# Performance work log

Measured on AMD Instinct MI355X. Metric: run time of the kernel, lower is better.

The kernel has to match this reference:

```python
import jax, jax.numpy as jnp
import numpy as np

B, C, H, W = 8, 256, 48, 48
G = 32  # num_groups
EPS = 1e-5


def setup_inputs() -> dict:
    key = jax.random.key(0)
    ks = jax.random.split(key, 9)
    s = 0.02
    return {
        "input": jax.random.normal(ks[0], (B, C, H, W), dtype=jnp.float32),
        "Wq": jax.random.normal(ks[1], (C, C), dtype=jnp.float32) * s,
        "bq": jnp.zeros((C,), dtype=jnp.float32),
        "Wk": jax.random.normal(ks[2], (C, C), dtype=jnp.float32) * s,
        "bk": jnp.zeros((C,), dtype=jnp.float32),
        "Wv": jax.random.normal(ks[3], (C, C), dtype=jnp.float32) * s,
        "bv": jnp.zeros((C,), dtype=jnp.float32),
        "gn_w": jnp.ones((C,), dtype=jnp.float32),
        "gn_b": jnp.zeros((C,), dtype=jnp.float32),
    }


def _group_norm(x, w, b):
    # x: [B, C, H, W] -> normalize per (group) over (C//G, H, W)
    n, c, h, wd = x.shape
    xg = x.reshape(n, G, c // G, h, wd)
    mean = jnp.mean(xg, axis=(2, 3, 4), keepdims=True)
    var = jnp.var(xg, axis=(2, 3, 4), keepdims=True)
    xg = (xg - mean) * jax.lax.rsqrt(var + EPS)
    x = xg.reshape(n, c, h, wd)
    return x * w[None, :, None, None] + b[None, :, None, None]


def _conv1x1(x, wgt, bias):
    # 1x1 conv == per-pixel channel GEMM. wgt: [C_out, C_in]
    return jnp.einsum('bchw,oc->bohw', x, wgt) + bias[None, :, None, None]


def reference(input, Wq, bq, Wk, bk, Wv, bv, gn_w, gn_b):
    x = _group_norm(input, gn_w, gn_b)
    q = _conv1x1(x, Wq, bq)
    k = _conv1x1(x, Wk, bk)
    v = _conv1x1(x, Wv, bv)
    d = q.shape[1]
    # energy[b,h,w,h',w'] = sum_c q[b,c,h,w] * k[b,c,h',w'] / sqrt(d)
    energy = jnp.einsum('bchw,bcef->bhwef', q, k) / jnp.sqrt(jnp.float32(d))
    n, h, w2 = energy.shape[0], energy.shape[1], energy.shape[2]
    energy = jax.nn.softmax(energy.reshape(n, h, w2, h * w2), axis=-1)
    energy = energy.reshape(n, h, w2, h, w2)
    # out[b,c,h,w] = sum_{h',w'} energy[b,h,w,h',w'] * v[b,c,h',w']
    out = jnp.einsum('bhwef,bcef->bchw', energy, v)
    return out
```

## Files before the change

kernel.cpp:

```cpp
#include <hip/hip_runtime.h>
#include <math.h>

#define NB 8
#define NC 256
#define NHW 2304
#define NG 32
#define CPG 8
#define GN_EPS 1e-5f
#define ATT_SCALE 0.0625f
#define XSTR 258

typedef __bf16 bf16x8 __attribute__((ext_vector_type(8)));
typedef __bf16 bf16x4 __attribute__((ext_vector_type(4)));
typedef float f32x4 __attribute__((ext_vector_type(4)));

#define MFMA(a, b, c) __builtin_amdgcn_mfma_f32_16x16x32_bf16(a, b, c, 0, 0, 0)

__device__ __forceinline__ void async_lds16(const void* g, void* l) {
  __builtin_amdgcn_global_load_lds(
      (const __attribute__((address_space(1))) void*)g,
      (__attribute__((address_space(3))) void*)l, 16, 0, 0);
}

__global__ __launch_bounds__(256) void k_prep(
    const float* __restrict__ x, const float* __restrict__ gn_w,
    const float* __restrict__ gn_b, float* __restrict__ scale,
    float* __restrict__ shift,
    const float* __restrict__ Wq, const float* __restrict__ Wk,
    const float* __restrict__ Wv, __bf16* __restrict__ Wqb,
    __bf16* __restrict__ Wkb, __bf16* __restrict__ Wvb) {
  __shared__ float red[8];
  int blk = blockIdx.x;
  if (blk >= 256) {
    int idx = blk - 256;
    int which = idx >> 6;
    const float* src = which == 0 ? Wq : (which == 1 ? Wk : Wv);
    __bf16* dst = which == 0 ? Wqb : (which == 1 ? Wkb : Wvb);
    int i = (idx & 63) * 256 + threadIdx.x;
    float4 v = ((const float4*)src)[i];
    bf16x4 o;
    o[0] = (__bf16)v.x; o[1] = (__bf16)v.y;
    o[2] = (__bf16)v.z; o[3] = (__bf16)v.w;
    ((bf16x4*)dst)[i] = o;
    return;
  }
  const float4* base = (const float4*)(x + (size_t)blk * CPG * NHW);
  const int n4 = CPG * NHW / 4;
  float s = 0.f, ss = 0.f;
  for (int i = threadIdx.x; i < n4; i += 256) {
    float4 v = base[i];
    s  += v.x + v.y + v.z + v.w;
    ss += v.x * v.x + v.y * v.y + v.z * v.z + v.w * v.w;
  }
  for (int off = 32; off > 0; off >>= 1) {
    s  += __shfl_down(s, off);
    ss += __shfl_down(ss, off);
  }
  int wv = threadIdx.x >> 6, ln = threadIdx.x & 63;
  if (ln == 0) { red[wv] = s; red[4 + wv] = ss; }
  __syncthreads();
  if (threadIdx.x < CPG) {
    float S  = red[0] + red[1] + red[2] + red[3];
    float SS = red[4] + red[5] + red[6] + red[7];
    const float inv_n = 1.f / (float)(CPG * NHW);
    float mean = S * inv_n;
    float var  = SS * inv_n - mean * mean;
    float rstd = rsqrtf(var + GN_EPS);
    int b = blk / NG, g = blk % NG;
    int c = g * CPG + threadIdx.x;
    float sc = gn_w[c] * rstd;
    scale[b * NC + c] = sc;
    shift[b * NC + c] = gn_b[c] - mean * sc;
  }
}

__global__ __launch_bounds__(256) void k_xnT(
    const float* __restrict__ x, const float* __restrict__ scale,
    const float* __restrict__ shift, __bf16* __restrict__ xnT) {
  __shared__ __bf16 t[64 * XSTR];
  int p0 = blockIdx.x * 64;
  int b = blockIdx.y;
  int w = threadIdx.x >> 6, lane = threadIdx.x & 63;
  const float* xb = x + (size_t)b * NC * NHW;
  const float* scb = scale + b * NC;
  const float* shb = shift + b * NC;
#pragma unroll 8
  for (int i = 0; i < 64; ++i) {
    int c = i * 4 + w;
    float v = xb[(size_t)c * NHW + p0 + lane] * scb[c] + shb[c];
    t[lane * XSTR + c] = (__bf16)v;
  }
  __syncthreads();
#pragma unroll
  for (int i = 0; i < 8; ++i) {
    int row = i * 8 + w * 2 + (lane >> 5);
    int c8 = (lane & 31) * 8;
    bf16x8 v8 = *(const bf16x8*)&t[row * XSTR + c8];
    *(bf16x8*)&xnT[((size_t)b * NHW + p0 + row) * NC + c8] = v8;
  }
}

__global__ __launch_bounds__(256) void k_qkv(
    const __bf16* __restrict__ xnT,
    const __bf16* __restrict__ Wqb, const __bf16* __restrict__ Wkb,
    const __bf16* __restrict__ Wvb,
    const float* __restrict__ bq, const float* __restrict__ bk,
    const float* __restrict__ bv,
    __bf16* __restrict__ qT, __bf16* __restrict__ kT,
    __bf16* __restrict__ vbuf) {
  __shared__ __bf16 tile[9216];
  int blk = blockIdx.x;
  int b = blk & 7;
  int r = blk >> 3;
  int oq = r & 3;
  int pg = r >> 2;
  int p0 = pg * 128, o0 = oq * 64;
  int tid = threadIdx.x;
  int w = tid >> 6, lane = tid & 63;
  int col = lane & 15, quad = lane >> 4;

  const __bf16* xrow =
      xnT + ((size_t)b * NHW + p0 + w * 32 + col) * NC + quad * 8;
  bf16x8 xf[2][8];
#pragma unroll
  for (int mt = 0; mt < 2; ++mt)
#pragma unroll
    for (int ks = 0; ks < 8; ++ks)
      xf[mt][ks] = *(const bf16x8*)(xrow + (size_t)mt * 16 * NC + ks * 32);

#pragma unroll
  for (int t = 0; t < 3; ++t) {
    const __bf16* W = t == 0 ? Wqb : (t == 1 ? Wkb : Wvb);
    const float* bias = t == 0 ? bq : (t == 1 ? bk : bv);
    f32x4 acc[2][4];
#pragma unroll
    for (int mt = 0; mt < 2; ++mt)
#pragma unroll
      for (int nt = 0; nt < 4; ++nt) acc[mt][nt] = (f32x4){0.f, 0.f, 0.f, 0.f};
#pragma unroll
    for (int nt = 0; nt < 4; ++nt) {
      const __bf16* wrow = W + ((size_t)(o0 + nt * 16 + col)) * NC + quad * 8;
#pragma unroll
      for (int ks = 0; ks < 8; ++ks) {
        bf16x8 wf = *(const bf16x8*)(wrow + ks * 32);
        acc[0][nt] = MFMA(xf[0][ks], wf, acc[0][nt]);
        acc[1][nt] = MFMA(xf[1][ks], wf, acc[1][nt]);
      }
    }
    if (t > 0) __syncthreads();
    if (t < 2) {
#pragma unroll
      for (int mt = 0; mt < 2; ++mt)
#pragma unroll
        for (int nt = 0; nt < 4; ++nt) {
          float bc = bias[o0 + nt * 16 + col];
#pragma unroll
          for (int reg = 0; reg < 4; ++reg) {
            int row = w * 32 + mt * 16 + quad * 4 + reg;
            tile[row * 72 + nt * 16 + col] = (__bf16)(acc[mt][nt][reg] + bc);
          }
        }
      __syncthreads();
      __bf16* dst = t == 0 ? qT : kT;
#pragma unroll
      for (int pass = 0; pass < 4; ++pass) {
        int unit = pass * 256 + tid;
        int row = unit >> 3, ch = unit & 7;
        bf16x8 v8 = *(const bf16x8*)&tile[row * 72 + ch * 8];
        *(bf16x8*)&dst[((size_t)b * NHW + p0 + row) * NC + o0 + ch * 8] = v8;
      }
    } else {
#pragma unroll
      for (int mt = 0; mt < 2; ++mt)
#pragma unroll
        for (int nt = 0; nt < 4; ++nt) {
          float bc = bias[o0 + nt * 16 + col];
#pragma unroll
          for (int reg = 0; reg < 4; ++reg) {
            int p = w * 32 + mt * 16 + quad * 4 + reg;
            tile[(nt * 16 + col) * 136 + p] = (__bf16)(acc[mt][nt][reg] + bc);
          }
        }
      __syncthreads();
#pragma unroll
      for (int pass = 0; pass < 4; ++pass) {
        int unit = pass * 256 + tid;
        int row = unit >> 4, ch = unit & 15;
        bf16x8 v8 = *(const bf16x8*)&tile[row * 136 + ch * 8];
        *(bf16x8*)&vbuf[((size_t)b * NC + o0 + row) * NHW + p0 + ch * 8] = v8;
      }
    }
  }
}

__global__ __launch_bounds__(256, 2) void k_fused(
    const __bf16* __restrict__ qT, const __bf16* __restrict__ kT,
    const __bf16* __restrict__ vbuf, float* __restrict__ out) {
  __shared__ __bf16 sk[64 * 256];
  __shared__ __bf16 sv[256 * 64];
  __shared__ __bf16 sp[64 * 64];
  __shared__ float slsum[2][64];

  int blk = blockIdx.x;
  int b = blk & 7;
  int qg = blk >> 3;
  int q0 = qg * 64;
  int tid = threadIdx.x;
  int w = tid >> 6, lane = tid & 63;
  int wm = w >> 1, wn = w & 1;
  int col = lane & 15, quad = lane >> 4;
  int c7 = col & 7;

  auto stage_kv = [&](int it2) {
    int k0 = it2 * 64;
    {
      int sub = lane >> 5, p5 = lane & 31;
#pragma unroll
      for (int j = 0; j < 8; ++j) {
        int r0 = w * 16 + j * 2;
        int rloc = r0 + sub;
        int g = p5 ^ (rloc & 7);
        async_lds16(kT + ((size_t)b * NHW + k0 + rloc) * NC + g * 8,
                    (void*)&sk[r0 * 256]);
      }
    }
    {
      int sub = lane >> 3, p3 = lane & 7;
#pragma unroll
      for (int j = 0; j < 8; ++j) {
        int r0 = w * 64 + j * 8;
        int rloc = r0 + sub;
        int g = p3 ^ (rloc & 7);
        async_lds16(vbuf + ((size_t)b * NC + rloc) * NHW + k0 + g * 8,
                    (void*)&sv[r0 * 64]);
      }
    }
  };

  const __bf16* qrow =
      qT + ((size_t)b * NHW + q0 + wn * 32 + col) * NC + quad * 8;
  bf16x8 qf[2][8];
#pragma unroll
  for (int nt = 0; nt < 2; ++nt)
#pragma unroll
    for (int ks = 0; ks < 8; ++ks)
      qf[nt][ks] = *(const bf16x8*)(qrow + (size_t)nt * 16 * NC + ks * 32);

  stage_kv(0);

  f32x4 acc[4][4];
#pragma unroll
  for (int mt = 0; mt < 4; ++mt)
#pragma unroll
    for (int nt = 0; nt < 4; ++nt) acc[mt][nt] = (f32x4){0.f, 0.f, 0.f, 0.f};
  float lsum_r[2] = {0.f, 0.f};

  for (int it = 0; it < 36; ++it) {
    __syncthreads();

    f32x4 sacc[2][2];
#pragma unroll
    for (int mt = 0; mt < 2; ++mt)
#pragma unroll
      for (int nt = 0; nt < 2; ++nt) sacc[mt][nt] = (f32x4){0.f, 0.f, 0.f, 0.f};
#pragma unroll
    for (int ks = 0; ks < 8; ++ks) {
#pragma unroll
      for (int mt = 0; mt < 2; ++mt) {
        int krow = wm * 32 + mt * 16 + col;
        bf16x8 kf = *(const bf16x8*)
            &sk[krow * 256 + (((ks * 4 + quad) ^ c7) << 3)];
        sacc[mt][0] = MFMA(kf, qf[0][ks], sacc[mt][0]);
        sacc[mt][1] = MFMA(kf, qf[1][ks], sacc[mt][1]);
      }
    }

#pragma unroll
    for (int nt = 0; nt < 2; ++nt) {
      float ps = 0.f;
      int q = wn * 32 + nt * 16 + col;
#pragma unroll
      for (int mt = 0; mt < 2; ++mt) {
        bf16x4 pk;
#pragma unroll
        for (int reg = 0; reg < 4; ++reg) {
          float e = __expf(sacc[mt][nt][reg] * ATT_SCALE);
          ps += e;
          pk[reg] = (__bf16)e;
        }
        int chunk = (wm * 4 + mt * 2 + (quad >> 1)) ^ c7;
        *(bf16x4*)&sp[q * 64 + chunk * 8 + (quad & 1) * 4] = pk;
      }
      ps += __shfl_xor(ps, 16);
      ps += __shfl_xor(ps, 32);
      lsum_r[nt] += ps;
    }

    __syncthreads();

    bf16x8 pf[4][2], vf[4][2];
#pragma unroll
    for (int nt = 0; nt < 4; ++nt) {
      int q = nt * 16 + col;
#pragma unroll
      for (int ks = 0; ks < 2; ++ks)
        pf[nt][ks] = *(const bf16x8*)
            &sp[q * 64 + (((ks * 4 + quad) ^ c7) << 3)];
    }
#pragma unroll
    for (int mt = 0; mt < 4; ++mt) {
      int crow = w * 64 + mt * 16 + col;
#pragma unroll
      for (int ks = 0; ks < 2; ++ks)
        vf[mt][ks] = *(const bf16x8*)
            &sv[crow * 64 + (((ks * 4 + quad) ^ c7) << 3)];
    }
    if (it < 35) {
      asm volatile("s_waitcnt lgkmcnt(0)" ::: "memory");
      __builtin_amdgcn_sched_barrier(0);
      stage_kv(it + 1);
    }

#pragma unroll
    for (int mt = 0; mt < 4; ++mt)
#pragma unroll
      for (int nt = 0; nt < 4; ++nt) {
        acc[mt][nt] = MFMA(vf[mt][0], pf[nt][0], acc[mt][nt]);
        acc[mt][nt] = MFMA(vf[mt][1], pf[nt][1], acc[mt][nt]);
      }
  }

  if (quad == 0) {
#pragma unroll
    for (int nt = 0; nt < 2; ++nt)
      slsum[wm][wn * 32 + nt * 16 + col] = lsum_r[nt];
  }
  __syncthreads();

  float* ob = out + (size_t)b * NC * NHW;
#pragma unroll
  for (int nt = 0; nt < 4; ++nt) {
    int q = nt * 16 + col;
    float inv = 1.f / (slsum[0][q] + slsum[1][q]);
#pragma unroll
    for (int mt = 0; mt < 4; ++mt) {
#pragma unroll
      for (int reg = 0; reg < 4; ++reg) {
        int c = w * 64 + mt * 16 + quad * 4 + reg;
        ob[(size_t)c * NHW + q0 + q] = acc[mt][nt][reg] * inv;
      }
    }
  }
}

extern "C" void kernel_launch(void* const* d_in, const int* in_sizes, int n_in,
                              void* d_out, int out_size, void* d_ws,
                              size_t ws_size, hipStream_t stream) {
  const float* x   = (const float*)d_in[0];
  const float* Wq  = (const float*)d_in[1];
  const float* bq  = (const float*)d_in[2];
  const float* Wk  = (const float*)d_in[3];
  const float* bk  = (const float*)d_in[4];
  const float* Wv  = (const float*)d_in[5];
  const float* bv  = (const float*)d_in[6];
  const float* gnw = (const float*)d_in[7];
  const float* gnb = (const float*)d_in[8];
  float* out = (float*)d_out;

  const size_t per = (size_t)NB * NC * NHW;
  const size_t psz = (size_t)NB * NHW * NHW * 2;
  char* wsb = (char*)d_ws;
  __bf16* qT   = (__bf16*)wsb;
  __bf16* kT   = (__bf16*)(wsb + per * 2);
  __bf16* vbuf = (__bf16*)(wsb + per * 4);
  __bf16* xnT  = (__bf16*)(wsb + per * 6);
  char* tail   = wsb + per * 6 + psz;
  __bf16* Wqb  = (__bf16*)tail;
  __bf16* Wkb  = Wqb + NC * NC;
  __bf16* Wvb  = Wkb + NC * NC;
  float* scale = (float*)(Wvb + NC * NC);
  float* shift = scale + NB * NC;

  hipLaunchKernelGGL(k_prep, dim3(448), dim3(256), 0, stream,
                     x, gnw, gnb, scale, shift, Wq, Wk, Wv, Wqb, Wkb, Wvb);
  hipLaunchKernelGGL(k_xnT, dim3(NHW / 64, NB), dim3(256), 0, stream,
                     x, scale, shift, xnT);
  hipLaunchKernelGGL(k_qkv, dim3(576), dim3(256), 0, stream,
                     xnT, Wqb, Wkb, Wvb, bq, bk, bv, qT, kT, vbuf);
  hipLaunchKernelGGL(k_fused, dim3(288), dim3(256), 0, stream,
                     qT, kT, vbuf, out);
}
```

Baseline: 243.6 us.

## Restructure fused attention: 32-query tiles, Q in LDS, K/V direct from global

The fused attention kernel now processes 32 queries per block instead of 64, doubling the grid to 576 blocks and raising the occupancy target to 3 blocks per CU. Q is staged once into swizzled LDS, while K and V fragments are loaded straight from global memory into registers each iteration instead of through async LDS staging. A double-buffered P tile replaces one of the two per-iteration block barriers. This aims to improve occupancy and cut LDS traffic and synchronisation, at the cost of reading K/V from global (or L2) more often, with no explicit prefetch overlap.

After: 329.2 us. +35.2%, slower.

```diff
diff --git a/kernel.cpp b/kernel.cpp
--- a/kernel.cpp
+++ b/kernel.cpp
@@ -15,12 +15,6 @@
 typedef float f32x4 __attribute__((ext_vector_type(4)));
 
 #define MFMA(a, b, c) __builtin_amdgcn_mfma_f32_16x16x32_bf16(a, b, c, 0, 0, 0)
-
-__device__ __forceinline__ void async_lds16(const void* g, void* l) {
-  __builtin_amdgcn_global_load_lds(
-      (const __attribute__((address_space(1))) void*)g,
-      (__attribute__((address_space(3))) void*)l, 16, 0, 0);
-}
 
 __global__ __launch_bounds__(256) void k_prep(
     const float* __restrict__ x, const float* __restrict__ gn_w,
@@ -193,155 +187,117 @@
   }
 }
 
-__global__ __launch_bounds__(256, 2) void k_fused(
+__global__ __launch_bounds__(256, 3) void k_fused(
     const __bf16* __restrict__ qT, const __bf16* __restrict__ kT,
     const __bf16* __restrict__ vbuf, float* __restrict__ out) {
-  __shared__ __bf16 sk[64 * 256];
-  __shared__ __bf16 sv[256 * 64];
-  __shared__ __bf16 sp[64 * 64];
-  __shared__ float slsum[2][64];
+  __shared__ __bf16 sq[32 * 256];
+  __shared__ __bf16 sp[2][32 * 64];
+  __shared__ float slsum[4][32];
 
   int blk = blockIdx.x;
   int b = blk & 7;
   int qg = blk >> 3;
-  int q0 = qg * 64;
+  int q0 = qg * 32;
   int tid = threadIdx.x;
   int w = tid >> 6, lane = tid & 63;
-  int wm = w >> 1, wn = w & 1;
   int col = lane & 15, quad = lane >> 4;
   int c7 = col & 7;
 
-  auto stage_kv = [&](int it2) {
-    int k0 = it2 * 64;
-    {
-      int sub = lane >> 5, p5 = lane & 31;
-#pragma unroll
-      for (int j = 0; j < 8; ++j) {
-        int r0 = w * 16 + j * 2;
-        int rloc = r0 + sub;
-        int g = p5 ^ (rloc & 7);
-        async_lds16(kT + ((size_t)b * NHW + k0 + rloc) * NC + g * 8,
-                    (void*)&sk[r0 * 256]);
-      }
-    }
-    {
-      int sub = lane >> 3, p3 = lane & 7;
-#pragma unroll
-      for (int j = 0; j < 8; ++j) {
-        int r0 = w * 64 + j * 8;
-        int rloc = r0 + sub;
-        int g = p3 ^ (rloc & 7);
-        async_lds16(vbuf + ((size_t)b * NC + rloc) * NHW + k0 + g * 8,
-                    (void*)&sv[r0 * 64]);
-      }
-    }
-  };
-
-  const __bf16* qrow =
-      qT + ((size_t)b * NHW + q0 + wn * 32 + col) * NC + quad * 8;
-  bf16x8 qf[2][8];
-#pragma unroll
-  for (int nt = 0; nt < 2; ++nt)
+  {
+    const __bf16* qb = qT + ((size_t)b * NHW + q0) * NC;
+#pragma unroll
+    for (int pass = 0; pass < 4; ++pass) {
+      int unit = pass * 256 + tid;
+      int q = unit >> 5, ch = unit & 31;
+      bf16x8 v8 = *(const bf16x8*)(qb + q * NC + ch * 8);
+      *(bf16x8*)&sq[q * 256 + ((ch ^ (q & 7)) << 3)] = v8;
+    }
+  }
+  __syncthreads();
+
+  const __bf16* kbase = kT + ((size_t)b * NHW + w * 16 + col) * NC + quad * 8;
+  const __bf16* vbase =
+      vbuf + ((size_t)b * NC + w * 64 + col) * NHW + quad * 8;
+
+  f32x4 acc[4][2];
+#pragma unroll
+  for (int mt = 0; mt < 4; ++mt)
+#pragma unroll
+    for (int nt = 0; nt < 2; ++nt) acc[mt][nt] = (f32x4){0.f, 0.f, 0.f, 0.f};
+  float lsum_r[2] = {0.f, 0.f};
+
+  for (int it = 0; it < 36; ++it) {
+    const __bf16* kp = kbase + (size_t)it * 64 * NC;
+    bf16x8 kf[8];
 #pragma unroll
     for (int ks = 0; ks < 8; ++ks)
-      qf[nt][ks] = *(const bf16x8*)(qrow + (size_t)nt * 16 * NC + ks * 32);
-
-  stage_kv(0);
-
-  f32x4 acc[4][4];
-#pragma unroll
-  for (int mt = 0; mt < 4; ++mt)
-#pragma unroll
-    for (int nt = 0; nt < 4; ++nt) acc[mt][nt] = (f32x4){0.f, 0.f, 0.f, 0.f};
-  float lsum_r[2] = {0.f, 0.f};
-
-  for (int it = 0; it < 36; ++it) {
-    __syncthreads();
-
-    f32x4 sacc[2][2];
-#pragma unroll
-    for (int mt = 0; mt < 2; ++mt)
-#pragma unroll
-      for (int nt = 0; nt < 2; ++nt) sacc[mt][nt] = (f32x4){0.f, 0.f, 0.f, 0.f};
+      kf[ks] = *(const bf16x8*)(kp + ks * 32);
+    const __bf16* vp = vbase + it * 64;
+    bf16x8 vf[4][2];
+#pragma unroll
+    for (int mt = 0; mt < 4; ++mt)
+#pragma unroll
+      for (int ks = 0; ks < 2; ++ks)
+        vf[mt][ks] = *(const bf16x8*)(vp + (size_t)mt * 16 * NHW + ks * 32);
+
+    f32x4 sacc[2];
+    sacc[0] = (f32x4){0.f, 0.f, 0.f, 0.f};
+    sacc[1] = (f32x4){0.f, 0.f, 0.f, 0.f};
 #pragma unroll
     for (int ks = 0; ks < 8; ++ks) {
-#pragma unroll
-      for (int mt = 0; mt < 2; ++mt) {
-        int krow = wm * 32 + mt * 16 + col;
-        bf16x8 kf = *(const bf16x8*)
-            &sk[krow * 256 + (((ks * 4 + quad) ^ c7) << 3)];
-        sacc[mt][0] = MFMA(kf, qf[0][ks], sacc[mt][0]);
-        sacc[mt][1] = MFMA(kf, qf[1][ks], sacc[mt][1]);
-      }
-    }
-
+      int sl = ((ks * 4 + quad) ^ c7) << 3;
+      bf16x8 q0f = *(const bf16x8*)&sq[col * 256 + sl];
+      bf16x8 q1f = *(const bf16x8*)&sq[(16 + col) * 256 + sl];
+      sacc[0] = MFMA(kf[ks], q0f, sacc[0]);
+      sacc[1] = MFMA(kf[ks], q1f, sacc[1]);
+    }
+
+    __bf16* spc = sp[it & 1];
+    int wrch = w * 2 + (quad >> 1);
 #pragma unroll
     for (int nt = 0; nt < 2; ++nt) {
       float ps = 0.f;
-      int q = wn * 32 + nt * 16 + col;
-#pragma unroll
-      for (int mt = 0; mt < 2; ++mt) {
-        bf16x4 pk;
-#pragma unroll
-        for (int reg = 0; reg < 4; ++reg) {
-          float e = __expf(sacc[mt][nt][reg] * ATT_SCALE);
-          ps += e;
-          pk[reg] = (__bf16)e;
-        }
-        int chunk = (wm * 4 + mt * 2 + (quad >> 1)) ^ c7;
-        *(bf16x4*)&sp[q * 64 + chunk * 8 + (quad & 1) * 4] = pk;
-      }
+      bf16x4 pk;
+#pragma unroll
+      for (int reg = 0; reg < 4; ++reg) {
+        float e = __expf(sacc[nt][reg] * ATT_SCALE);
+        ps += e;
+        pk[reg] = (__bf16)e;
+      }
+      int q = nt * 16 + col;
+      *(bf16x4*)&spc[q * 64 + ((wrch ^ c7) << 3) + (quad & 1) * 4] = pk;
       ps += __shfl_xor(ps, 16);
       ps += __shfl_xor(ps, 32);
       lsum_r[nt] += ps;
     }
-
-    __syncthreads();
-
-    bf16x8 pf[4][2], vf[4][2];
-#pragma unroll
-    for (int nt = 0; nt < 4; ++nt) {
-      int q = nt * 16 + col;
-#pragma unroll
-      for (int ks = 0; ks < 2; ++ks)
-        pf[nt][ks] = *(const bf16x8*)
-            &sp[q * 64 + (((ks * 4 + quad) ^ c7) << 3)];
-    }
-#pragma unroll
-    for (int mt = 0; mt < 4; ++mt) {
-      int crow = w * 64 + mt * 16 + col;
-#pragma unroll
-      for (int ks = 0; ks < 2; ++ks)
-        vf[mt][ks] = *(const bf16x8*)
-            &sv[crow * 64 + (((ks * 4 + quad) ^ c7) << 3)];
-    }
-    if (it < 35) {
-      asm volatile("s_waitcnt lgkmcnt(0)" ::: "memory");
-      __builtin_amdgcn_sched_barrier(0);
-      stage_kv(it + 1);
-    }
-
-#pragma unroll
-    for (int mt = 0; mt < 4; ++mt)
-#pragma unroll
-      for (int nt = 0; nt < 4; ++nt) {
-        acc[mt][nt] = MFMA(vf[mt][0], pf[nt][0], acc[mt][nt]);
-        acc[mt][nt] = MFMA(vf[mt][1], pf[nt][1], acc[mt][nt]);
-      }
+    asm volatile("s_waitcnt lgkmcnt(0)" ::: "memory");
+    __builtin_amdgcn_s_barrier();
+    __builtin_amdgcn_sched_barrier(0x26);
+
+#pragma unroll
+    for (int nt = 0; nt < 2; ++nt) {
+      int qrow = (nt * 16 + col) * 64;
+      bf16x8 pf0 = *(const bf16x8*)&spc[qrow + (((quad) ^ c7) << 3)];
+      bf16x8 pf1 = *(const bf16x8*)&spc[qrow + (((4 + quad) ^ c7) << 3)];
+#pragma unroll
+      for (int mt = 0; mt < 4; ++mt) {
+        acc[mt][nt] = MFMA(vf[mt][0], pf0, acc[mt][nt]);
+        acc[mt][nt] = MFMA(vf[mt][1], pf1, acc[mt][nt]);
+      }
+    }
   }
 
   if (quad == 0) {
-#pragma unroll
-    for (int nt = 0; nt < 2; ++nt)
-      slsum[wm][wn * 32 + nt * 16 + col] = lsum_r[nt];
+    slsum[w][col] = lsum_r[0];
+    slsum[w][16 + col] = lsum_r[1];
   }
   __syncthreads();
 
   float* ob = out + (size_t)b * NC * NHW;
 #pragma unroll
-  for (int nt = 0; nt < 4; ++nt) {
+  for (int nt = 0; nt < 2; ++nt) {
     int q = nt * 16 + col;
-    float inv = 1.f / (slsum[0][q] + slsum[1][q]);
+    float inv = 1.f / (slsum[0][q] + slsum[1][q] + slsum[2][q] + slsum[3][q]);
 #pragma unroll
     for (int mt = 0; mt < 4; ++mt) {
 #pragma unroll
@@ -387,6 +343,6 @@
                      x, scale, shift, xnT);
   hipLaunchKernelGGL(k_qkv, dim3(576), dim3(256), 0, stream,
                      xnT, Wqb, Wkb, Wvb, bq, bk, bv, qT, kT, vbuf);
-  hipLaunchKernelGGL(k_fused, dim3(288), dim3(256), 0, stream,
+  hipLaunchKernelGGL(k_fused, dim3(576), dim3(256), 0, stream,
                      qT, kT, vbuf, out);
 }
```

## Split attention over two key halves and combine partials in separate kernel

Applied to the files above, without the earlier changes.

Each query tile of the fused attention kernel now processes only half of the key/value sequence, which doubles the grid from 288 to 576 blocks. Each block writes unnormalized fp32 partial outputs and row sums to workspace, and a new elementwise kernel adds the two halves and divides. The intent is more parallelism and better spreading of work across the CUs. The cost is an extra kernel launch and writing then rereading two fp32 partial output tensors.

Result: slower. 255.4 us (+4.8%).

```diff
diff --git a/kernel.cpp b/kernel.cpp
--- a/kernel.cpp
+++ b/kernel.cpp
@@ -195,7 +195,8 @@
 
 __global__ __launch_bounds__(256, 2) void k_fused(
     const __bf16* __restrict__ qT, const __bf16* __restrict__ kT,
-    const __bf16* __restrict__ vbuf, float* __restrict__ out) {
+    const __bf16* __restrict__ vbuf, float* __restrict__ opart,
+    float* __restrict__ lpart) {
   __shared__ __bf16 sk[64 * 256];
   __shared__ __bf16 sv[256 * 64];
   __shared__ __bf16 sp[64 * 64];
@@ -203,7 +204,9 @@
 
   int blk = blockIdx.x;
   int b = blk & 7;
-  int qg = blk >> 3;
+  int r = blk >> 3;
+  int kh = r & 1;
+  int qg = r >> 1;
   int q0 = qg * 64;
   int tid = threadIdx.x;
   int w = tid >> 6, lane = tid & 63;
@@ -212,7 +215,7 @@
   int c7 = col & 7;
 
   auto stage_kv = [&](int it2) {
-    int k0 = it2 * 64;
+    int k0 = (kh * 18 + it2) * 64;
     {
       int sub = lane >> 5, p5 = lane & 31;
 #pragma unroll
@@ -255,7 +258,7 @@
     for (int nt = 0; nt < 4; ++nt) acc[mt][nt] = (f32x4){0.f, 0.f, 0.f, 0.f};
   float lsum_r[2] = {0.f, 0.f};
 
-  for (int it = 0; it < 36; ++it) {
+  for (int it = 0; it < 18; ++it) {
     __syncthreads();
 
     f32x4 sacc[2][2];
@@ -315,7 +318,7 @@
         vf[mt][ks] = *(const bf16x8*)
             &sv[crow * 64 + (((ks * 4 + quad) ^ c7) << 3)];
     }
-    if (it < 35) {
+    if (it < 17) {
       asm volatile("s_waitcnt lgkmcnt(0)" ::: "memory");
       __builtin_amdgcn_sched_barrier(0);
       stage_kv(it + 1);
@@ -337,20 +340,44 @@
   }
   __syncthreads();
 
-  float* ob = out + (size_t)b * NC * NHW;
+  float* opb = opart + (size_t)kh * NB * NC * NHW + (size_t)b * NC * NHW;
+  float* lpb = lpart + (size_t)kh * NB * NHW + (size_t)b * NHW + q0;
 #pragma unroll
   for (int nt = 0; nt < 4; ++nt) {
     int q = nt * 16 + col;
-    float inv = 1.f / (slsum[0][q] + slsum[1][q]);
+    float lsumv = slsum[0][q] + slsum[1][q];
+    if (w == 0 && quad == 0) lpb[q] = lsumv;
 #pragma unroll
     for (int mt = 0; mt < 4; ++mt) {
 #pragma unroll
       for (int reg = 0; reg < 4; ++reg) {
         int c = w * 64 + mt * 16 + quad * 4 + reg;
-        ob[(size_t)c * NHW + q0 + q] = acc[mt][nt][reg] * inv;
-      }
-    }
-  }
+        opb[(size_t)c * NHW + q0 + q] = acc[mt][nt][reg];
+      }
+    }
+  }
+}
+
+__global__ __launch_bounds__(256) void k_comb(
+    const float* __restrict__ opart, const float* __restrict__ lpart,
+    float* __restrict__ out) {
+  int i = blockIdx.x * 256 + threadIdx.x;
+  const float4* o0 = (const float4*)opart;
+  const float4* o1 = (const float4*)(opart + (size_t)NB * NC * NHW);
+  float4 a = o0[i], c = o1[i];
+  int flat = i * 4;
+  int q = flat % NHW;
+  int b = flat / (NC * NHW);
+  const float4* l0 = (const float4*)lpart;
+  const float4* l1 = (const float4*)(lpart + NB * NHW);
+  int li = (b * NHW + q) >> 2;
+  float4 s = l0[li], t = l1[li];
+  float4 rr;
+  rr.x = (a.x + c.x) / (s.x + t.x);
+  rr.y = (a.y + c.y) / (s.y + t.y);
+  rr.z = (a.z + c.z) / (s.z + t.z);
+  rr.w = (a.w + c.w) / (s.w + t.w);
+  ((float4*)out)[i] = rr;
 }
 
 extern "C" void kernel_launch(void* const* d_in, const int* in_sizes, int n_in,
@@ -368,13 +395,14 @@
   float* out = (float*)d_out;
 
   const size_t per = (size_t)NB * NC * NHW;
-  const size_t psz = (size_t)NB * NHW * NHW * 2;
   char* wsb = (char*)d_ws;
   __bf16* qT   = (__bf16*)wsb;
   __bf16* kT   = (__bf16*)(wsb + per * 2);
   __bf16* vbuf = (__bf16*)(wsb + per * 4);
   __bf16* xnT  = (__bf16*)(wsb + per * 6);
-  char* tail   = wsb + per * 6 + psz;
+  float* opart = (float*)(wsb + per * 6);
+  float* lpart = (float*)(wsb + per * 14);
+  char* tail   = wsb + per * 14 + (size_t)2 * NB * NHW * 4;
   __bf16* Wqb  = (__bf16*)tail;
   __bf16* Wkb  = Wqb + NC * NC;
   __bf16* Wvb  = Wkb + NC * NC;
@@ -387,6 +415,8 @@
                      x, scale, shift, xnT);
   hipLaunchKernelGGL(k_qkv, dim3(576), dim3(256), 0, stream,
                      xnT, Wqb, Wkb, Wvb, bq, bk, bv, qT, kT, vbuf);
-  hipLaunchKernelGGL(k_fused, dim3(288), dim3(256), 0, stream,
-                     qT, kT, vbuf, out);
-}
+  hipLaunchKernelGGL(k_fused, dim3(576), dim3(256), 0, stream,
+                     qT, kT, vbuf, opart, lpart);
+  hipLaunchKernelGGL(k_comb, dim3(4608), dim3(256), 0, stream,
+                     opart, lpart, out);
+}
```

## Fuse group-norm transpose into QKV projection kernel, dropping xnT buffer

Applied to the files above, without the earlier changes.

Merges the normalize-and-transpose kernel into the QKV GEMM kernel. Each block now normalizes a 64-pixel tile into shared memory and computes all 256 output channels for Q, K and V from it. This removes the global write and re-read of the bf16 normalized activations plus one launch. The cost is fewer blocks (288 instead of 576), more shared memory per block and larger accumulator register use (16 tiles), which may lower occupancy.

New measurement: 331.0 us. +35.9%, slower.

```diff
diff --git a/kernel.cpp b/kernel.cpp
--- a/kernel.cpp
+++ b/kernel.cpp
@@ -74,120 +74,96 @@
   }
 }
 
-__global__ __launch_bounds__(256) void k_xnT(
+__global__ __launch_bounds__(256) void k_qkvn(
     const float* __restrict__ x, const float* __restrict__ scale,
-    const float* __restrict__ shift, __bf16* __restrict__ xnT) {
-  __shared__ __bf16 t[64 * XSTR];
-  int p0 = blockIdx.x * 64;
-  int b = blockIdx.y;
-  int w = threadIdx.x >> 6, lane = threadIdx.x & 63;
-  const float* xb = x + (size_t)b * NC * NHW;
-  const float* scb = scale + b * NC;
-  const float* shb = shift + b * NC;
-#pragma unroll 8
-  for (int i = 0; i < 64; ++i) {
-    int c = i * 4 + w;
-    float v = xb[(size_t)c * NHW + p0 + lane] * scb[c] + shb[c];
-    t[lane * XSTR + c] = (__bf16)v;
-  }
-  __syncthreads();
-#pragma unroll
-  for (int i = 0; i < 8; ++i) {
-    int row = i * 8 + w * 2 + (lane >> 5);
-    int c8 = (lane & 31) * 8;
-    bf16x8 v8 = *(const bf16x8*)&t[row * XSTR + c8];
-    *(bf16x8*)&xnT[((size_t)b * NHW + p0 + row) * NC + c8] = v8;
-  }
-}
-
-__global__ __launch_bounds__(256) void k_qkv(
-    const __bf16* __restrict__ xnT,
+    const float* __restrict__ shift,
     const __bf16* __restrict__ Wqb, const __bf16* __restrict__ Wkb,
     const __bf16* __restrict__ Wvb,
     const float* __restrict__ bq, const float* __restrict__ bk,
     const float* __restrict__ bv,
     __bf16* __restrict__ qT, __bf16* __restrict__ kT,
     __bf16* __restrict__ vbuf) {
-  __shared__ __bf16 tile[9216];
+  __shared__ __bf16 t[64 * XSTR];
+  __shared__ __bf16 ob[256 * 72];
   int blk = blockIdx.x;
   int b = blk & 7;
-  int r = blk >> 3;
-  int oq = r & 3;
-  int pg = r >> 2;
-  int p0 = pg * 128, o0 = oq * 64;
+  int pg = blk >> 3;
+  int p0 = pg * 64;
   int tid = threadIdx.x;
   int w = tid >> 6, lane = tid & 63;
   int col = lane & 15, quad = lane >> 4;
 
-  const __bf16* xrow =
-      xnT + ((size_t)b * NHW + p0 + w * 32 + col) * NC + quad * 8;
-  bf16x8 xf[2][8];
-#pragma unroll
-  for (int mt = 0; mt < 2; ++mt)
-#pragma unroll
-    for (int ks = 0; ks < 8; ++ks)
-      xf[mt][ks] = *(const bf16x8*)(xrow + (size_t)mt * 16 * NC + ks * 32);
-
-#pragma unroll
-  for (int t = 0; t < 3; ++t) {
-    const __bf16* W = t == 0 ? Wqb : (t == 1 ? Wkb : Wvb);
-    const float* bias = t == 0 ? bq : (t == 1 ? bk : bv);
-    f32x4 acc[2][4];
-#pragma unroll
-    for (int mt = 0; mt < 2; ++mt)
-#pragma unroll
-      for (int nt = 0; nt < 4; ++nt) acc[mt][nt] = (f32x4){0.f, 0.f, 0.f, 0.f};
-#pragma unroll
-    for (int nt = 0; nt < 4; ++nt) {
-      const __bf16* wrow = W + ((size_t)(o0 + nt * 16 + col)) * NC + quad * 8;
+  {
+    const float* xb = x + (size_t)b * NC * NHW;
+    const float* scb = scale + b * NC;
+    const float* shb = shift + b * NC;
+#pragma unroll 8
+    for (int i = 0; i < 64; ++i) {
+      int c = i * 4 + w;
+      float v = xb[(size_t)c * NHW + p0 + lane] * scb[c] + shb[c];
+      t[lane * XSTR + c] = (__bf16)v;
+    }
+  }
+  __syncthreads();
+
+  bf16x8 xf[8];
+#pragma unroll
+  for (int ks = 0; ks < 8; ++ks)
+    xf[ks] = *(const bf16x8*)&t[(w * 16 + col) * XSTR + ks * 32 + quad * 8];
+
+#pragma unroll
+  for (int t3 = 0; t3 < 3; ++t3) {
+    const __bf16* W = t3 == 0 ? Wqb : (t3 == 1 ? Wkb : Wvb);
+    const float* bias = t3 == 0 ? bq : (t3 == 1 ? bk : bv);
+    f32x4 acc[16];
+#pragma unroll
+    for (int nt = 0; nt < 16; ++nt) acc[nt] = (f32x4){0.f, 0.f, 0.f, 0.f};
+#pragma unroll
+    for (int nt = 0; nt < 16; ++nt) {
+      const __bf16* wrow = W + ((size_t)(nt * 16 + col)) * NC + quad * 8;
 #pragma unroll
       for (int ks = 0; ks < 8; ++ks) {
         bf16x8 wf = *(const bf16x8*)(wrow + ks * 32);
-        acc[0][nt] = MFMA(xf[0][ks], wf, acc[0][nt]);
-        acc[1][nt] = MFMA(xf[1][ks], wf, acc[1][nt]);
-      }
-    }
-    if (t > 0) __syncthreads();
-    if (t < 2) {
-#pragma unroll
-      for (int mt = 0; mt < 2; ++mt)
-#pragma unroll
-        for (int nt = 0; nt < 4; ++nt) {
-          float bc = bias[o0 + nt * 16 + col];
-#pragma unroll
-          for (int reg = 0; reg < 4; ++reg) {
-            int row = w * 32 + mt * 16 + quad * 4 + reg;
-            tile[row * 72 + nt * 16 + col] = (__bf16)(acc[mt][nt][reg] + bc);
-          }
+        acc[nt] = MFMA(xf[ks], wf, acc[nt]);
+      }
+    }
+    if (t3 > 0) __syncthreads();
+    if (t3 < 2) {
+#pragma unroll
+      for (int nt = 0; nt < 16; ++nt) {
+        float bc = bias[nt * 16 + col];
+#pragma unroll
+        for (int reg = 0; reg < 4; ++reg) {
+          int row = w * 16 + quad * 4 + reg;
+          ob[row * 264 + nt * 16 + col] = (__bf16)(acc[nt][reg] + bc);
         }
+      }
       __syncthreads();
-      __bf16* dst = t == 0 ? qT : kT;
-#pragma unroll
-      for (int pass = 0; pass < 4; ++pass) {
+      __bf16* dst = t3 == 0 ? qT : kT;
+#pragma unroll
+      for (int pass = 0; pass < 8; ++pass) {
+        int unit = pass * 256 + tid;
+        int row = unit >> 5, ch = unit & 31;
+        bf16x8 v8 = *(const bf16x8*)&ob[row * 264 + ch * 8];
+        *(bf16x8*)&dst[((size_t)b * NHW + p0 + row) * NC + ch * 8] = v8;
+      }
+    } else {
+#pragma unroll
+      for (int nt = 0; nt < 16; ++nt) {
+        float bc = bias[nt * 16 + col];
+#pragma unroll
+        for (int reg = 0; reg < 4; ++reg) {
+          int p = w * 16 + quad * 4 + reg;
+          ob[(nt * 16 + col) * 72 + p] = (__bf16)(acc[nt][reg] + bc);
+        }
+      }
+      __syncthreads();
+#pragma unroll
+      for (int pass = 0; pass < 8; ++pass) {
         int unit = pass * 256 + tid;
         int row = unit >> 3, ch = unit & 7;
-        bf16x8 v8 = *(const bf16x8*)&tile[row * 72 + ch * 8];
-        *(bf16x8*)&dst[((size_t)b * NHW + p0 + row) * NC + o0 + ch * 8] = v8;
-      }
-    } else {
-#pragma unroll
-      for (int mt = 0; mt < 2; ++mt)
-#pragma unroll
-        for (int nt = 0; nt < 4; ++nt) {
-          float bc = bias[o0 + nt * 16 + col];
-#pragma unroll
-          for (int reg = 0; reg < 4; ++reg) {
-            int p = w * 32 + mt * 16 + quad * 4 + reg;
-            tile[(nt * 16 + col) * 136 + p] = (__bf16)(acc[mt][nt][reg] + bc);
-          }
-        }
-      __syncthreads();
-#pragma unroll
-      for (int pass = 0; pass < 4; ++pass) {
-        int unit = pass * 256 + tid;
-        int row = unit >> 4, ch = unit & 15;
-        bf16x8 v8 = *(const bf16x8*)&tile[row * 136 + ch * 8];
-        *(bf16x8*)&vbuf[((size_t)b * NC + o0 + row) * NHW + p0 + ch * 8] = v8;
+        bf16x8 v8 = *(const bf16x8*)&ob[row * 72 + ch * 8];
+        *(bf16x8*)&vbuf[((size_t)b * NC + row) * NHW + p0 + ch * 8] = v8;
       }
     }
   }
@@ -368,13 +344,11 @@
   float* out = (float*)d_out;
 
   const size_t per = (size_t)NB * NC * NHW;
-  const size_t psz = (size_t)NB * NHW * NHW * 2;
   char* wsb = (char*)d_ws;
   __bf16* qT   = (__bf16*)wsb;
   __bf16* kT   = (__bf16*)(wsb + per * 2);
   __bf16* vbuf = (__bf16*)(wsb + per * 4);
-  __bf16* xnT  = (__bf16*)(wsb + per * 6);
-  char* tail   = wsb + per * 6 + psz;
+  char* tail   = wsb + per * 6;
   __bf16* Wqb  = (__bf16*)tail;
   __bf16* Wkb  = Wqb + NC * NC;
   __bf16* Wvb  = Wkb + NC * NC;
@@ -383,10 +357,9 @@
 
   hipLaunchKernelGGL(k_prep, dim3(448), dim3(256), 0, stream,
                      x, gnw, gnb, scale, shift, Wq, Wk, Wv, Wqb, Wkb, Wvb);
-  hipLaunchKernelGGL(k_xnT, dim3(NHW / 64, NB), dim3(256), 0, stream,
-                     x, scale, shift, xnT);
-  hipLaunchKernelGGL(k_qkv, dim3(576), dim3(256), 0, stream,
-                     xnT, Wqb, Wkb, Wvb, bq, bk, bv, qT, kT, vbuf);
+  hipLaunchKernelGGL(k_qkvn, dim3(288), dim3(256), 0, stream,
+                     x, scale, shift, Wqb, Wkb, Wvb, bq, bk, bv,
+                     qT, kT, vbuf);
   hipLaunchKernelGGL(k_fused, dim3(288), dim3(256), 0, stream,
                      qT, kT, vbuf, out);
 }
```
